# Kernel tuning notes

Measured on AMD Instinct MI355X. Metric: run time of the kernel, lower is better.

Reference implementation:

```python
import jax, jax.numpy as jnp
import numpy as np

V, E, H, B, S, K, L = 32000, 512, 1024, 16, 128, 15, 1


def setup_inputs() -> dict:
    key = jax.random.key(0)
    ks = jax.random.split(key, 12)
    s = 0.02
    W_emb = jax.random.normal(ks[0], (V, E), jnp.float32) * s
    W_emb = W_emb.at[0].set(0.0)  # padding_idx=0
    return {
        "input_ids": jax.random.randint(ks[1], (B, S), 0, V),
        "hidden": jnp.zeros((L, B, H), jnp.float32),
        "stop_indicators": jax.random.randint(ks[2], (B, S), 0, 2),
        "W_emb": W_emb,
        "W_ih": jax.random.normal(ks[3], (H, E), jnp.float32) * s,
        "b_ih": jax.random.normal(ks[4], (H,), jnp.float32) * s,
        "W_hh": jax.random.normal(ks[5], (H, H), jnp.float32) * s,
        "b_hh": jax.random.normal(ks[6], (H,), jnp.float32) * s,
        "W_dec": jax.random.normal(ks[7], (V, H), jnp.float32) * s,
        "b_dec": jax.random.normal(ks[8], (V,), jnp.float32) * s,
        "beta": jax.random.uniform(ks[9], (K, V), jnp.float32),
        "theta": jax.random.uniform(ks[10], (K,), jnp.float32),
    }


def reference(input_ids, hidden, stop_indicators, W_emb, W_ih, b_ih, W_hh, b_hh,
              W_dec, b_dec, beta, theta):
    # Embedding lookup: [B, S, E]
    emb = W_emb[input_ids]
    xs = jnp.swapaxes(emb, 0, 1)  # [S, B, E] time-major for scan
    h0 = hidden[0]                # [B, H]

    # Elman RNN (tanh), single layer, batch_first semantics
    def step(h, x):
        h_new = jnp.tanh(x @ W_ih.T + b_ih + h @ W_hh.T + b_hh)
        return h_new, h_new

    hT, outs = jax.lax.scan(step, h0, xs)      # outs: [S, B, H]
    output = jnp.swapaxes(outs, 0, 1)          # [B, S, H]

    decoded = output @ W_dec.T + b_dec         # [B, S, V]

    # Topic additions: single fused GEMV theta @ beta (replaces per-vocab loop)
    topic_additions = theta @ beta             # [V]
    stop_mask = (stop_indicators == 0).astype(decoded.dtype)[..., None]  # [B,S,1]
    decoded = decoded + topic_additions * stop_mask

    return decoded, hT[None]  # hidden back as [layers=1, B, H]
```

## Files before the change

### kernel.cpp

```cpp
#include <hip/hip_runtime.h>
#include <stdint.h>

#define V_ 32000
#define E_ 512
#define H_ 1024
#define B_ 16
#define S_ 128
#define K_ 15

typedef float floatx4 __attribute__((ext_vector_type(4)));
typedef short shortx8 __attribute__((ext_vector_type(8)));
typedef __bf16 bf16x8 __attribute__((ext_vector_type(8)));

static __device__ __forceinline__ unsigned short f2b(float f) {
  union { float f; uint32_t u; } v; v.f = f;
  uint32_t u = v.u;
  u += 0x7FFFu + ((u >> 16) & 1u);
  return (unsigned short)(u >> 16);
}

static __device__ __forceinline__ shortx8 cvt8(floatx4 a, floatx4 b) {
  shortx8 r;
  r[0] = (short)f2b(a[0]); r[1] = (short)f2b(a[1]);
  r[2] = (short)f2b(a[2]); r[3] = (short)f2b(a[3]);
  r[4] = (short)f2b(b[0]); r[5] = (short)f2b(b[1]);
  r[6] = (short)f2b(b[2]); r[7] = (short)f2b(b[3]);
  return r;
}

static __device__ __forceinline__ floatx4 mfma_bf16(shortx8 a, shortx8 b, floatx4 c) {
  return __builtin_amdgcn_mfma_f32_16x16x32_bf16(
      __builtin_bit_cast(bf16x8, a), __builtin_bit_cast(bf16x8, b), c, 0, 0, 0);
}


__global__ void k_zero(int* __restrict__ p, int n) {
  int i = blockIdx.x * blockDim.x + threadIdx.x;
  if (i < n) p[i] = 0;
}

__global__ void k_topic(const float* __restrict__ beta, const float* __restrict__ theta,
                        float* __restrict__ topic) {
  int n = blockIdx.x * blockDim.x + threadIdx.x;
  float s = 0.f;
#pragma unroll
  for (int k = 0; k < K_; ++k) s += theta[k] * beta[k * V_ + n];
  topic[n] = s;
}

__global__ void k_cvt(const float* __restrict__ src, unsigned short* __restrict__ dst) {
  size_t i = (size_t)(blockIdx.x * blockDim.x + threadIdx.x) * 8;
  floatx4 f0 = *(const floatx4*)(src + i);
  floatx4 f1 = *(const floatx4*)(src + i + 4);
  *(shortx8*)(dst + i) = cvt8(f0, f1);
}

__global__ __launch_bounds__(256, 2) void k_gemm_pre(
    const int* __restrict__ ids, const float* __restrict__ W_emb,
    const float* __restrict__ W_ih, const float* __restrict__ b_ih,
    const float* __restrict__ b_hh, float* __restrict__ pre) {
  __shared__ unsigned short As[128 * 72];
  __shared__ unsigned short Bs[128 * 72];
  const int tid = threadIdx.x;
  const int gn0 = blockIdx.x * 128;
  const int gm0 = blockIdx.y * 128;
  const int wave = tid >> 6, lane = tid & 63;
  const int wm = (wave >> 1) * 64, wn = (wave & 1) * 64;
  const int lr = lane & 15, lg = lane >> 4;

  floatx4 acc[4][4];
#pragma unroll
  for (int i = 0; i < 4; ++i)
#pragma unroll
    for (int j = 0; j < 4; ++j) acc[i][j] = (floatx4)0.0f;

  for (int k0 = 0; k0 < E_; k0 += 64) {
#pragma unroll
    for (int c = 0; c < 4; ++c) {
      int q = c * 256 + tid;
      int row = q >> 3, kc = (q & 7) * 8;
      int m = gm0 + row;
      int id = ids[(m & 15) * S_ + (m >> 4)];
      const float* ga = W_emb + (size_t)id * E_ + k0 + kc;
      floatx4 a0 = *(const floatx4*)ga;
      floatx4 a1 = *(const floatx4*)(ga + 4);
      *(shortx8*)&As[row * 72 + kc] = cvt8(a0, a1);
      const float* gb = W_ih + (size_t)(gn0 + row) * E_ + k0 + kc;
      floatx4 c0 = *(const floatx4*)gb;
      floatx4 c1 = *(const floatx4*)(gb + 4);
      *(shortx8*)&Bs[row * 72 + kc] = cvt8(c0, c1);
    }
    __syncthreads();
#pragma unroll
    for (int ks = 0; ks < 64; ks += 32) {
      shortx8 af[4], bfr[4];
#pragma unroll
      for (int i = 0; i < 4; ++i)
        af[i] = *(const shortx8*)&As[(wm + i * 16 + lr) * 72 + ks + lg * 8];
#pragma unroll
      for (int j = 0; j < 4; ++j)
        bfr[j] = *(const shortx8*)&Bs[(wn + j * 16 + lr) * 72 + ks + lg * 8];
#pragma unroll
      for (int i = 0; i < 4; ++i)
#pragma unroll
        for (int j = 0; j < 4; ++j) acc[i][j] = mfma_bf16(af[i], bfr[j], acc[i][j]);
    }
    __syncthreads();
  }
#pragma unroll
  for (int i = 0; i < 4; ++i) {
#pragma unroll
    for (int r = 0; r < 4; ++r) {
      int m = gm0 + wm + i * 16 + lg * 4 + r;
#pragma unroll
      for (int j = 0; j < 4; ++j) {
        int n = gn0 + wn + j * 16 + lr;
        pre[(size_t)m * H_ + n] = acc[i][j][r] + b_ih[n] + b_hh[n];
      }
    }
  }
}

__global__ __launch_bounds__(256, 1) void k_rnn(
    const float* __restrict__ hidden0, const float* __restrict__ W_hh,
    const float* __restrict__ pre, unsigned short* __restrict__ hb,
    unsigned short* __restrict__ act,
    float* __restrict__ hT_out,
    int* __restrict__ bar) {
  const int tid = threadIdx.x, bid = blockIdx.x;
  const int lane = tid & 63, wave = tid >> 6;
  const int lr = lane & 15, lg = lane >> 4;
  const int nn = bid * 64 + wave * 16 + lr;

  shortx8 bfr[32];
#pragma unroll
  for (int s = 0; s < 32; ++s) {
    const float* g = W_hh + (size_t)nn * H_ + s * 32 + lg * 8;
    floatx4 f0 = *(const floatx4*)g;
    floatx4 f1 = *(const floatx4*)(g + 4);
    bfr[s] = cvt8(f0, f1);
  }

  {
    int gt = (bid * 256 + tid) * 4;
#pragma unroll
    for (int u = 0; u < 4; ++u) {
      int e = gt + u;
      int b = e >> 10, n = e & 1023;
      hb[(((n >> 5) * 64 + ((n >> 3) & 3) * 16 + b) << 3) + (n & 7)] = f2b(hidden0[e]);
    }
  }

  __syncthreads();
  if (tid == 0) {
    __threadfence();
    __hip_atomic_fetch_add(&bar[0], 1, __ATOMIC_ACQ_REL, __HIP_MEMORY_SCOPE_AGENT);
    while (__hip_atomic_load(&bar[0], __ATOMIC_ACQUIRE, __HIP_MEMORY_SCOPE_AGENT) < 16)
      __builtin_amdgcn_s_sleep(1);
  }
  __syncthreads();

  const int sft = (((nn >> 5) * 64 + ((nn >> 3) & 3) * 16) << 3) + (nn & 7);

  for (int t = 0; t < S_; ++t) {
    const unsigned short* hcur = hb + (t & 1) * (B_ * H_);
    unsigned short* hnxt = hb + ((t + 1) & 1) * (B_ * H_);

    float prer[4];
#pragma unroll
    for (int r = 0; r < 4; ++r)
      prer[r] = pre[((size_t)t * B_ + lg * 4 + r) * H_ + nn];

    floatx4 a0 = (floatx4)0.f, a1 = (floatx4)0.f, a2 = (floatx4)0.f, a3 = (floatx4)0.f;
#pragma unroll
    for (int s = 0; s < 32; s += 4) {
      shortx8 f0 = *(const shortx8*)&hcur[((s + 0) * 64 + lane) * 8];
      shortx8 f1 = *(const shortx8*)&hcur[((s + 1) * 64 + lane) * 8];
      shortx8 f2 = *(const shortx8*)&hcur[((s + 2) * 64 + lane) * 8];
      shortx8 f3 = *(const shortx8*)&hcur[((s + 3) * 64 + lane) * 8];
      a0 = mfma_bf16(f0, bfr[s + 0], a0);
      a1 = mfma_bf16(f1, bfr[s + 1], a1);
      a2 = mfma_bf16(f2, bfr[s + 2], a2);
      a3 = mfma_bf16(f3, bfr[s + 3], a3);
    }
    floatx4 acc = (a0 + a1) + (a2 + a3);

#pragma unroll
    for (int r = 0; r < 4; ++r) {
      int b = lg * 4 + r;
      float h = tanhf(acc[r] + prer[r]);
      unsigned short h16 = f2b(h);
      hnxt[sft + b * 8] = h16;
      act[((size_t)b * S_ + t) * H_ + nn] = h16;
      if (t == S_ - 1) hT_out[b * H_ + nn] = h;
    }

    if (t < S_ - 1) {
      __syncthreads();
      if (tid == 0) {
        __threadfence();
        __hip_atomic_fetch_add(&bar[(t + 1) * 32], 1, __ATOMIC_ACQ_REL,
                               __HIP_MEMORY_SCOPE_AGENT);
        while (__hip_atomic_load(&bar[(t + 1) * 32], __ATOMIC_ACQUIRE,
                                 __HIP_MEMORY_SCOPE_AGENT) < 16)
          __builtin_amdgcn_s_sleep(1);
      }
      __syncthreads();
    }
  }
}

__global__ __launch_bounds__(256, 2) void k_gemm_dec(
    const unsigned short* __restrict__ A, const unsigned short* __restrict__ Bw,
    const float* __restrict__ b_dec, const float* __restrict__ topic,
    const int* __restrict__ stop, float* __restrict__ out) {
  __shared__ unsigned short As[128 * 72];
  __shared__ unsigned short Bs[128 * 72];
  const int tid = threadIdx.x;
  const int gn0 = blockIdx.x * 128;
  const int gm0 = blockIdx.y * 128;
  const int wave = tid >> 6, lane = tid & 63;
  const int wm = (wave >> 1) * 64, wn = (wave & 1) * 64;
  const int lr = lane & 15, lg = lane >> 4;

  floatx4 acc[4][4];
#pragma unroll
  for (int i = 0; i < 4; ++i)
#pragma unroll
    for (int j = 0; j < 4; ++j) acc[i][j] = (floatx4)0.0f;

  for (int k0 = 0; k0 < H_; k0 += 64) {
#pragma unroll
    for (int c = 0; c < 4; ++c) {
      int q = c * 256 + tid;
      int row = q >> 3, kc = (q & 7) * 8;
      *(shortx8*)&As[row * 72 + kc] =
          *(const shortx8*)(A + (size_t)(gm0 + row) * H_ + k0 + kc);
      *(shortx8*)&Bs[row * 72 + kc] =
          *(const shortx8*)(Bw + (size_t)(gn0 + row) * H_ + k0 + kc);
    }
    __syncthreads();
#pragma unroll
    for (int ks = 0; ks < 64; ks += 32) {
      shortx8 af[4], bfr[4];
#pragma unroll
      for (int i = 0; i < 4; ++i)
        af[i] = *(const shortx8*)&As[(wm + i * 16 + lr) * 72 + ks + lg * 8];
#pragma unroll
      for (int j = 0; j < 4; ++j)
        bfr[j] = *(const shortx8*)&Bs[(wn + j * 16 + lr) * 72 + ks + lg * 8];
#pragma unroll
      for (int i = 0; i < 4; ++i)
#pragma unroll
        for (int j = 0; j < 4; ++j) acc[i][j] = mfma_bf16(af[i], bfr[j], acc[i][j]);
    }
    __syncthreads();
  }
#pragma unroll
  for (int i = 0; i < 4; ++i) {
#pragma unroll
    for (int r = 0; r < 4; ++r) {
      int m = gm0 + wm + i * 16 + lg * 4 + r;
      float msk = (stop[m] == 0) ? 1.f : 0.f;
      size_t base = (size_t)m * V_;
#pragma unroll
      for (int j = 0; j < 4; ++j) {
        int n = gn0 + wn + j * 16 + lr;
        out[base + n] = acc[i][j][r] + b_dec[n] + topic[n] * msk;
      }
    }
  }
}

extern "C" void kernel_launch(void* const* d_in, const int* in_sizes, int n_in,
                              void* d_out, int out_size, void* d_ws, size_t ws_size,
                              hipStream_t stream) {
  (void)in_sizes; (void)n_in; (void)out_size; (void)ws_size;
  const int*   ids    = (const int*)d_in[0];
  const float* hidden = (const float*)d_in[1];
  const int*   stop   = (const int*)d_in[2];
  const float* W_emb  = (const float*)d_in[3];
  const float* W_ih   = (const float*)d_in[4];
  const float* b_ih   = (const float*)d_in[5];
  const float* W_hh   = (const float*)d_in[6];
  const float* b_hh   = (const float*)d_in[7];
  const float* W_dec  = (const float*)d_in[8];
  const float* b_dec  = (const float*)d_in[9];
  const float* beta   = (const float*)d_in[10];
  const float* theta  = (const float*)d_in[11];
  float* out = (float*)d_out;

  char* ws = (char*)d_ws;
  size_t off = 0;
  auto alloc = [&](size_t bytes) -> void* {
    void* p = ws + off;
    off = (off + bytes + 255) & ~(size_t)255;
    return p;
  };
  int* bar = (int*)alloc(16384 * sizeof(int));
  float* topic = (float*)alloc((size_t)V_ * 4);
  float* pre = (float*)alloc((size_t)B_ * S_ * H_ * 4);
  unsigned short* act = (unsigned short*)alloc((size_t)B_ * S_ * H_ * 2);
  unsigned short* hb = (unsigned short*)alloc((size_t)2 * B_ * H_ * 2);
  unsigned short* wdec16 = (unsigned short*)alloc((size_t)V_ * H_ * 2);

  k_zero<<<dim3(32), dim3(512), 0, stream>>>(bar, 16384);
  k_topic<<<dim3(V_ / 256), dim3(256), 0, stream>>>(beta, theta, topic);
  k_cvt<<<dim3((V_ * H_) / (256 * 8)), dim3(256), 0, stream>>>(W_dec, wdec16);
  k_gemm_pre<<<dim3(H_ / 128, (B_ * S_) / 128), dim3(256), 0, stream>>>(
      ids, W_emb, W_ih, b_ih, b_hh, pre);
  k_rnn<<<dim3(16), dim3(256), 0, stream>>>(hidden, W_hh, pre, hb, act,
                                            out + (size_t)B_ * S_ * V_, bar);
  k_gemm_dec<<<dim3(V_ / 128, (B_ * S_) / 128), dim3(256), 0, stream>>>(
      act, wdec16, b_dec, topic, stop, out);
}
```

Baseline: 1.243 ms.

## Replace RNN atomic-counter grid barrier with per-block flags and prefetch pre

```diff
diff --git a/kernel.cpp b/kernel.cpp
--- a/kernel.cpp
+++ b/kernel.cpp
@@ -121,16 +121,16 @@
   }
 }
 
-__global__ __launch_bounds__(256, 1) void k_rnn(
+__global__ __launch_bounds__(128, 1) void k_rnn(
     const float* __restrict__ hidden0, const float* __restrict__ W_hh,
     const float* __restrict__ pre, unsigned short* __restrict__ hb,
     unsigned short* __restrict__ act,
     float* __restrict__ hT_out,
-    int* __restrict__ bar) {
+    int* __restrict__ flags) {
   const int tid = threadIdx.x, bid = blockIdx.x;
   const int lane = tid & 63, wave = tid >> 6;
   const int lr = lane & 15, lg = lane >> 4;
-  const int nn = bid * 64 + wave * 16 + lr;
+  const int nn = bid * 32 + wave * 16 + lr;
 
   shortx8 bfr[32];
 #pragma unroll
@@ -142,7 +142,7 @@
   }
 
   {
-    int gt = (bid * 256 + tid) * 4;
+    int gt = (bid * 128 + tid) * 4;
 #pragma unroll
     for (int u = 0; u < 4; ++u) {
       int e = gt + u;
@@ -151,25 +151,28 @@
     }
   }
 
+  __builtin_amdgcn_fence(__ATOMIC_RELEASE, "workgroup");
   __syncthreads();
-  if (tid == 0) {
-    __threadfence();
-    __hip_atomic_fetch_add(&bar[0], 1, __ATOMIC_ACQ_REL, __HIP_MEMORY_SCOPE_AGENT);
-    while (__hip_atomic_load(&bar[0], __ATOMIC_ACQUIRE, __HIP_MEMORY_SCOPE_AGENT) < 16)
+  if (tid == 0)
+    __hip_atomic_store(&flags[bid * 32], 1, __ATOMIC_RELEASE, __HIP_MEMORY_SCOPE_AGENT);
+
+  float prer[4], prer2[4];
+#pragma unroll
+  for (int r = 0; r < 4; ++r) prer[r] = pre[((size_t)(lg * 4 + r)) * H_ + nn];
+
+  if (tid < 32) {
+    while (__hip_atomic_load(&flags[tid * 32], __ATOMIC_RELAXED,
+                             __HIP_MEMORY_SCOPE_AGENT) < 1)
       __builtin_amdgcn_s_sleep(1);
   }
   __syncthreads();
+  __builtin_amdgcn_fence(__ATOMIC_ACQUIRE, "agent");
 
   const int sft = (((nn >> 5) * 64 + ((nn >> 3) & 3) * 16) << 3) + (nn & 7);
 
   for (int t = 0; t < S_; ++t) {
     const unsigned short* hcur = hb + (t & 1) * (B_ * H_);
     unsigned short* hnxt = hb + ((t + 1) & 1) * (B_ * H_);
-
-    float prer[4];
-#pragma unroll
-    for (int r = 0; r < 4; ++r)
-      prer[r] = pre[((size_t)t * B_ + lg * 4 + r) * H_ + nn];
 
     floatx4 a0 = (floatx4)0.f, a1 = (floatx4)0.f, a2 = (floatx4)0.f, a3 = (floatx4)0.f;
 #pragma unroll
@@ -196,16 +199,23 @@
     }
 
     if (t < S_ - 1) {
+      __builtin_amdgcn_fence(__ATOMIC_RELEASE, "workgroup");
       __syncthreads();
-      if (tid == 0) {
-        __threadfence();
-        __hip_atomic_fetch_add(&bar[(t + 1) * 32], 1, __ATOMIC_ACQ_REL,
-                               __HIP_MEMORY_SCOPE_AGENT);
-        while (__hip_atomic_load(&bar[(t + 1) * 32], __ATOMIC_ACQUIRE,
-                                 __HIP_MEMORY_SCOPE_AGENT) < 16)
+      if (tid == 0)
+        __hip_atomic_store(&flags[bid * 32], t + 2, __ATOMIC_RELEASE,
+                           __HIP_MEMORY_SCOPE_AGENT);
+#pragma unroll
+      for (int r = 0; r < 4; ++r)
+        prer2[r] = pre[((size_t)(t + 1) * B_ + lg * 4 + r) * H_ + nn];
+      if (tid < 32) {
+        while (__hip_atomic_load(&flags[tid * 32], __ATOMIC_RELAXED,
+                                 __HIP_MEMORY_SCOPE_AGENT) < t + 2)
           __builtin_amdgcn_s_sleep(1);
       }
       __syncthreads();
+      __builtin_amdgcn_fence(__ATOMIC_ACQUIRE, "agent");
+#pragma unroll
+      for (int r = 0; r < 4; ++r) prer[r] = prer2[r];
     }
   }
 }
@@ -297,20 +307,20 @@
     off = (off + bytes + 255) & ~(size_t)255;
     return p;
   };
-  int* bar = (int*)alloc(16384 * sizeof(int));
+  int* flags = (int*)alloc(16384 * sizeof(int));
   float* topic = (float*)alloc((size_t)V_ * 4);
   float* pre = (float*)alloc((size_t)B_ * S_ * H_ * 4);
   unsigned short* act = (unsigned short*)alloc((size_t)B_ * S_ * H_ * 2);
   unsigned short* hb = (unsigned short*)alloc((size_t)2 * B_ * H_ * 2);
   unsigned short* wdec16 = (unsigned short*)alloc((size_t)V_ * H_ * 2);
 
-  k_zero<<<dim3(32), dim3(512), 0, stream>>>(bar, 16384);
+  k_zero<<<dim3(32), dim3(512), 0, stream>>>(flags, 16384);
   k_topic<<<dim3(V_ / 256), dim3(256), 0, stream>>>(beta, theta, topic);
   k_cvt<<<dim3((V_ * H_) / (256 * 8)), dim3(256), 0, stream>>>(W_dec, wdec16);
   k_gemm_pre<<<dim3(H_ / 128, (B_ * S_) / 128), dim3(256), 0, stream>>>(
       ids, W_emb, W_ih, b_ih, b_hh, pre);
-  k_rnn<<<dim3(16), dim3(256), 0, stream>>>(hidden, W_hh, pre, hb, act,
-                                            out + (size_t)B_ * S_ * V_, bar);
+  k_rnn<<<dim3(32), dim3(128), 0, stream>>>(hidden, W_hh, pre, hb, act,
+                                            out + (size_t)B_ * S_ * V_, flags);
   k_gemm_dec<<<dim3(V_ / 128, (B_ * S_) / 128), dim3(256), 0, stream>>>(
       act, wdec16, b_dec, topic, stop, out);
 }
```

Result: slower. 1.285 ms (+3.4%).
